# Performance work log

Hardware: AMD Instinct MI355X
Metric: run time of the kernel (lower is better)

Reference implementation:

```python
import jax, jax.numpy as jnp
import numpy as np

MARGIN = 0.2
NEG_SENTINEL = -1e30


def setup_inputs() -> dict:
    key = jax.random.key(0)
    k1, k2 = jax.random.split(key)
    batch_reprs = jax.random.normal(k1, (4096, 128), dtype=jnp.float32)
    batch_labels = jax.random.randint(k2, (4096,), 0, 512, dtype=jnp.int64 if jax.config.jax_enable_x64 else jnp.int32)
    return {"batch_reprs": batch_reprs, "batch_labels": batch_labels}


def _loss(batch_reprs, batch_labels):
    # class match matrix (self-similarity kept, as in original)
    match = (batch_labels[:, None] == batch_labels[None, :]).astype(batch_reprs.dtype)  # [B,B]

    # pairwise euclidean distance (squared=False), sim = -dist
    sq = jnp.sum(batch_reprs * batch_reprs, axis=1)
    d2 = jnp.maximum(sq[:, None] + sq[None, :] - 2.0 * (batch_reprs @ batch_reprs.T), 0.0)
    zero = (d2 == 0.0).astype(batch_reprs.dtype)
    dist = jnp.sqrt(d2 + zero * 1e-16) * (1.0 - zero)
    sim_hat = -dist + (1.0 - match) * MARGIN  # use_margin=True

    # rank positions via double argsort (descending)
    order = jnp.argsort(-sim_hat, axis=1)
    rank = jnp.argsort(order, axis=1).astype(sim_hat.dtype) + 1.0  # [B,B], 1-based ranks

    k = jnp.sum(match, axis=1, keepdims=True)                      # n_pos per row, [B,1]
    fp = (match < 1.0) & (rank <= k)                               # false positives
    fp_num = jnp.sum(fp, axis=1, keepdims=True).astype(sim_hat.dtype)
    fn = (match > 0.0) & (rank > k)                                # false negatives

    n = sim_hat.shape[1]
    # per-row top-(fp_num) false negatives by sim_hat, vectorized via masked sort
    fn_scores = jnp.where(fn, sim_hat, NEG_SENTINEL)
    idx = jnp.argsort(-fn_scores, axis=1)
    fn_sorted = jnp.take_along_axis(sim_hat, idx, axis=1)
    fn_ranks = jnp.take_along_axis(rank, idx, axis=1)
    fn_mask_sorted = jnp.take_along_axis(fn, idx, axis=1)
    sel = (jnp.arange(n)[None, :] < fp_num) & fn_mask_sorted       # top fp_num entries

    # weighted margins (rows with fp_num==0 contribute 0 automatically)
    fp_term = jnp.sum(jnp.where(fp, sim_hat * (0.5 + (k - rank + 1.0) / k * 0.5), 0.0))
    fn_term = jnp.sum(jnp.where(sel, fn_sorted * (0.5 + (fn_ranks - k) / (n - k) * 0.5), 0.0))
    return fp_term - fn_term


def reference(batch_reprs, batch_labels):
    return _loss(batch_reprs, batch_labels)
```

## Files before the change

### kernel.cpp

```cpp
#include <hip/hip_runtime.h>
#include <cstdint>
#include <cstddef>

#define B 4096
#define D 128
#define MARGIN_F 0.2f
#define CW 256
#define ROWS 16
#define SSTR 4104

typedef short bf16x8 __attribute__((ext_vector_type(8)));
typedef float f32x4 __attribute__((ext_vector_type(4)));
typedef uint32_t u32x4 __attribute__((ext_vector_type(4)));

__device__ __forceinline__ uint32_t xform_key(float f) {
    uint32_t u = __float_as_uint(f);
    return u ^ (uint32_t)((((int32_t)u) >> 31) | 0x80000000);
}
__device__ __forceinline__ float unxform16(uint32_t k16) {
    uint32_t u = k16 << 16;
    u = (u & 0x80000000u) ? (u ^ 0x80000000u) : ~u;
    return __uint_as_float(u);
}
__device__ __forceinline__ unsigned short f2bf(float f) {
    uint32_t u = __float_as_uint(f);
    return (unsigned short)((u + 0x7FFFu + ((u >> 16) & 1u)) >> 16);
}

__global__ __launch_bounds__(256) void prep_kernel(const float* __restrict__ R,
                                                   float* __restrict__ sq,
                                                   unsigned short* __restrict__ Rb,
                                                   float* __restrict__ out) {
    if (blockIdx.x == 0 && threadIdx.x == 0) out[0] = 0.0f;
    int wave = threadIdx.x >> 6;
    int lane = threadIdx.x & 63;
    int row  = blockIdx.x * 4 + wave;
    const float2* R2 = (const float2*)R + (size_t)row * (D / 2);
    float2 v = R2[lane];
    ushort2 o; o.x = f2bf(v.x); o.y = f2bf(v.y);
    *(ushort2*)(Rb + (size_t)row * D + lane * 2) = o;
    float s = v.x * v.x + v.y * v.y;
#pragma unroll
    for (int off = 32; off > 0; off >>= 1) s += __shfl_down(s, off);
    if (lane == 0) sq[row] = s;
}

__global__ __launch_bounds__(512) void fused_loss(const unsigned short* __restrict__ Rb,
                                                  const float* __restrict__ sq,
                                                  const int* __restrict__ labels,
                                                  float* __restrict__ out) {
    __shared__ unsigned short S[ROWS * SSTR];
    __shared__ uint32_t cand_c[ROWS][CW];
    __shared__ int cnt[ROWS];

    const int tid  = threadIdx.x;
    const int wid  = tid >> 6, lane = tid & 63;
    const int q    = lane >> 4, t = lane & 15;
    const int r0   = blockIdx.x * ROWS;

    if (tid < ROWS) cnt[tid] = 0;

    bf16x8 af[4];
    const unsigned short* baseA = Rb + (size_t)(r0 + t) * D + q * 8;
#pragma unroll
    for (int kq = 0; kq < 4; ++kq)
        af[kq] = *(const bf16x8*)(baseA + kq * 32);

    float sqa[4]; int la[4];
#pragma unroll
    for (int rr = 0; rr < 4; ++rr) {
        sqa[rr] = sq[r0 + q * 4 + rr];
        la[rr]  = labels[r0 + q * 4 + rr];
    }

    for (int i = 0; i < 32; ++i) {
        const int jt  = wid * 32 + i;
        const int col = jt * 16 + t;
        const unsigned short* baseB = Rb + (size_t)col * D + q * 8;
        bf16x8 bfr[4];
#pragma unroll
        for (int kq = 0; kq < 4; ++kq)
            bfr[kq] = *(const bf16x8*)(baseB + kq * 32);
        f32x4 acc = (f32x4)0.0f;
#pragma unroll
        for (int kq = 0; kq < 4; ++kq)
            acc = __builtin_amdgcn_mfma_f32_16x16x32_bf16(af[kq], bfr[kq], acc, 0, 0, 0);

        const float sqc = sq[col];
        const int   lc  = labels[col];
#pragma unroll
        for (int rr = 0; rr < 4; ++rr) {
            float g  = acc[rr];
            float d2 = fmaxf(sqa[rr] + sqc - 2.0f * g, 0.0f);
            float dist = (d2 > 0.0f) ? sqrtf(d2) : 0.0f;
            float s = -dist + ((la[rr] == lc) ? 0.0f : MARGIN_F);
            uint32_t key = xform_key(s);
            S[(q * 4 + rr) * SSTR + col] = (unsigned short)((key + 0x8000u) >> 16);
        }
    }
    __syncthreads();

    float facc = 0.0f;
    const int4* lv = (const int4*)labels;

    for (int rr2 = 0; rr2 < 2; ++rr2) {
        const int row  = wid * 2 + rr2;
        const int grow = r0 + row;
        const int li   = labels[grow];

        u32x4 kv[8];
#pragma unroll
        for (int qq = 0; qq < 8; ++qq)
            kv[qq] = *(u32x4*)(&S[row * SSTR + (qq * 64 + lane) * 8]);

        uint64_t mbits = 0;
        uint32_t t1 = 0, t2 = 0;
#pragma unroll
        for (int qq = 0; qq < 8; ++qq) {
            const int lb = (qq * 64 + lane) * 2;
            int4 la4 = lv[lb], lc4 = lv[lb + 1];
            uint32_t u[8] = {kv[qq].x & 0xFFFFu, kv[qq].x >> 16,
                             kv[qq].y & 0xFFFFu, kv[qq].y >> 16,
                             kv[qq].z & 0xFFFFu, kv[qq].z >> 16,
                             kv[qq].w & 0xFFFFu, kv[qq].w >> 16};
#pragma unroll
            for (int c = 0; c < 8; ++c) {
                uint32_t mn = min(t1, u[c]);
                t1 = max(t1, u[c]);
                t2 = max(t2, mn);
            }
            mbits |= (uint64_t)(la4.x == li) << (qq * 8 + 0);
            mbits |= (uint64_t)(la4.y == li) << (qq * 8 + 1);
            mbits |= (uint64_t)(la4.z == li) << (qq * 8 + 2);
            mbits |= (uint64_t)(la4.w == li) << (qq * 8 + 3);
            mbits |= (uint64_t)(lc4.x == li) << (qq * 8 + 4);
            mbits |= (uint64_t)(lc4.y == li) << (qq * 8 + 5);
            mbits |= (uint64_t)(lc4.z == li) << (qq * 8 + 6);
            mbits |= (uint64_t)(lc4.w == li) << (qq * 8 + 7);
        }

        int kloc = __popcll(mbits);
#pragma unroll
        for (int off = 32; off > 0; off >>= 1) kloc += __shfl_xor(kloc, off);
        const int k = kloc;
        const float kf = (float)k;

        const int kneed = min(k, 128);
        uint32_t T = 0;
#pragma unroll
        for (int b = 15; b >= 0; --b) {
            uint32_t g = T | (1u << b);
            int c = __popcll(__ballot(t1 >= g)) + __popcll(__ballot(t2 >= g));
            if (c >= kneed) T = g;
        }
        const uint32_t combT = T << 12;

#pragma unroll
        for (int qq = 0; qq < 8; ++qq) {
            uint32_t u[8] = {kv[qq].x & 0xFFFFu, kv[qq].x >> 16,
                             kv[qq].y & 0xFFFFu, kv[qq].y >> 16,
                             kv[qq].z & 0xFFFFu, kv[qq].z >> 16,
                             kv[qq].w & 0xFFFFu, kv[qq].w >> 16};
            int jb = (qq * 64 + lane) * 8;
#pragma unroll
            for (int c = 0; c < 8; ++c) {
                int e = qq * 8 + c;
                uint32_t m = (uint32_t)((mbits >> e) & 1);
                if (u[c] >= T || m) {
                    int p = atomicAdd(&cnt[row], 1);
                    if (p < CW)
                        cand_c[row][p] = (u[c] << 12) | (uint32_t)(4095 - (jb + c)) | (m << 31);
                }
            }
        }
        const int ncand = min(cnt[row], CW);

        for (int s = lane; s < ncand; s += 64) {
            uint32_t cs = cand_c[row][s];
            uint32_t comb = cs & 0x7FFFFFFFu;
            int m = (int)(cs >> 31);
            if (comb >= combT) {
                int c2 = 0;
                for (int c = 0; c < ncand; ++c)
                    c2 += ((cand_c[row][c] & 0x7FFFFFFFu) > comb) ? 1 : 0;
                int rank = 1 + c2;
                float v = unxform16(comb >> 12);
                if (!m && rank <= k)
                    facc += v * (0.5f + ((kf - (float)rank + 1.0f) / kf) * 0.5f);
                else if (m && rank > k)
                    facc -= v * (0.5f + (((float)rank - kf) / (float)(B - k)) * 0.5f);
            }
        }

        uint32_t p0 = 0xFFFFFFFFu, p1 = 0xFFFFFFFFu, p2 = 0xFFFFFFFFu, p3 = 0xFFFFFFFFu;
        int np = 0;
        for (int c = 0; c <= ncand; ++c) {
            bool flushit = (c == ncand);
            if (!flushit) {
                uint32_t cc_ = cand_c[row][c];
                if ((cc_ & 0x80000000u) && (cc_ & 0x7FFFFFFFu) < combT) {
                    uint32_t comb = cc_ & 0x7FFFFFFFu;
                    if (np == 0) p0 = comb; else if (np == 1) p1 = comb;
                    else if (np == 2) p2 = comb; else p3 = comb;
                    ++np;
                    flushit = (np == 4);
                }
            }
            if (flushit && np > 0) {
                int c0 = 0, c1 = 0, c2 = 0, c3 = 0;
#pragma unroll
                for (int qq = 0; qq < 8; ++qq) {
                    uint32_t u[8] = {kv[qq].x & 0xFFFFu, kv[qq].x >> 16,
                                     kv[qq].y & 0xFFFFu, kv[qq].y >> 16,
                                     kv[qq].z & 0xFFFFu, kv[qq].z >> 16,
                                     kv[qq].w & 0xFFFFu, kv[qq].w >> 16};
                    int jb = (qq * 64 + lane) * 8;
#pragma unroll
                    for (int cc = 0; cc < 8; ++cc) {
                        uint32_t comb_e = (u[cc] << 12) | (uint32_t)(4095 - (jb + cc));
                        c0 += (comb_e > p0) ? 1 : 0;
                        c1 += (comb_e > p1) ? 1 : 0;
                        c2 += (comb_e > p2) ? 1 : 0;
                        c3 += (comb_e > p3) ? 1 : 0;
                    }
                }
#pragma unroll
                for (int off = 32; off > 0; off >>= 1) {
                    c0 += __shfl_xor(c0, off); c1 += __shfl_xor(c1, off);
                    c2 += __shfl_xor(c2, off); c3 += __shfl_xor(c3, off);
                }
                if (lane == 0) {
                    int rk[4] = {1 + c0, 1 + c1, 1 + c2, 1 + c3};
                    uint32_t pp[4] = {p0, p1, p2, p3};
                    for (int ii = 0; ii < np; ++ii) {
                        float v = unxform16(pp[ii] >> 12);
                        facc -= v * (0.5f + (((float)rk[ii] - kf) / (float)(B - k)) * 0.5f);
                    }
                }
                p0 = p1 = p2 = p3 = 0xFFFFFFFFu;
                np = 0;
            }
        }
    }

#pragma unroll
    for (int off = 32; off > 0; off >>= 1) facc += __shfl_xor(facc, off);
    if (lane == 0) atomicAdd(out, facc);
}

extern "C" void kernel_launch(void* const* d_in, const int* in_sizes, int n_in,
                              void* d_out, int out_size, void* d_ws, size_t ws_size,
                              hipStream_t stream) {
    const float* R      = (const float*)d_in[0];
    const int*   labels = (const int*)d_in[1];
    float* out = (float*)d_out;

    float*          sq = (float*)d_ws;
    unsigned short* Rb = (unsigned short*)((char*)d_ws + 16 * 1024);

    hipLaunchKernelGGL(prep_kernel, dim3(B / 4), dim3(256), 0, stream, R, sq, Rb, out);
    hipLaunchKernelGGL(fused_loss, dim3(B / ROWS), dim3(512), 0, stream,
                       Rb, sq, labels, out);
}
```

Before: 135.7 us.

## Register-blocked candidate ranking and ballot-based batching of false-negative rank queries

The candidate rank pass is rewritten so each lane holds four candidates in registers and scans the shared candidate list once with vectorized 128-bit loads, rather than doing a scalar scan per candidate. The candidate buffer is zeroed first so the list can be padded to a multiple of 8 without reading garbage. Low-score false negatives are now collected with wave ballots and shuffles and ranked eight at a time against the full row, instead of being found by a serial scan and ranked four at a time. This cuts LDS traffic and the number of full-row passes, at the cost of higher register pressure and a small zero-initialization step.

```diff
diff --git a/kernel.cpp b/kernel.cpp
--- a/kernel.cpp
+++ b/kernel.cpp
@@ -58,6 +58,12 @@
     const int q    = lane >> 4, t = lane & 15;
     const int r0   = blockIdx.x * ROWS;
 
+    {
+        uint32_t* cz = &cand_c[0][0];
+#pragma unroll
+        for (int c = 0; c < (ROWS * CW) / 512; ++c)
+            cz[tid + c * 512] = 0u;
+    }
     if (tid < ROWS) cnt[tid] = 0;
 
     bf16x8 af[4];
@@ -175,72 +181,108 @@
         }
         const int ncand = min(cnt[row], CW);
 
-        for (int s = lane; s < ncand; s += 64) {
-            uint32_t cs = cand_c[row][s];
-            uint32_t comb = cs & 0x7FFFFFFFu;
-            int m = (int)(cs >> 31);
-            if (comb >= combT) {
-                int c2 = 0;
-                for (int c = 0; c < ncand; ++c)
-                    c2 += ((cand_c[row][c] & 0x7FFFFFFFu) > comb) ? 1 : 0;
-                int rank = 1 + c2;
-                float v = unxform16(comb >> 12);
-                if (!m && rank <= k)
+        uint32_t cr0 = cand_c[row][lane];
+        uint32_t cr1 = cand_c[row][lane + 64];
+        uint32_t cr2 = cand_c[row][lane + 128];
+        uint32_t cr3 = cand_c[row][lane + 192];
+        uint32_t mycomb[4] = {cr0 & 0x7FFFFFFFu, cr1 & 0x7FFFFFFFu,
+                              cr2 & 0x7FFFFFFFu, cr3 & 0x7FFFFFFFu};
+        int mym[4]  = {(int)(cr0 >> 31), (int)(cr1 >> 31),
+                       (int)(cr2 >> 31), (int)(cr3 >> 31)};
+        int myok[4] = {lane < ncand, lane + 64 < ncand,
+                       lane + 128 < ncand, lane + 192 < ncand};
+        int myc[4]  = {0, 0, 0, 0};
+
+        const int npad = (ncand + 7) & ~7;
+        for (int c0i = 0; c0i < npad; c0i += 8) {
+            u32x4 a = *(const u32x4*)&cand_c[row][c0i];
+            u32x4 b = *(const u32x4*)&cand_c[row][c0i + 4];
+            uint32_t vv[8] = {a.x, a.y, a.z, a.w, b.x, b.y, b.z, b.w};
+#pragma unroll
+            for (int e = 0; e < 8; ++e) {
+                uint32_t vm = vv[e] & 0x7FFFFFFFu;
+#pragma unroll
+                for (int j = 0; j < 4; ++j)
+                    myc[j] += (vm > mycomb[j]) ? 1 : 0;
+            }
+        }
+
+#pragma unroll
+        for (int j = 0; j < 4; ++j) {
+            if (myok[j] && mycomb[j] >= combT) {
+                int rank = 1 + myc[j];
+                float v = unxform16(mycomb[j] >> 12);
+                if (!mym[j] && rank <= k)
                     facc += v * (0.5f + ((kf - (float)rank + 1.0f) / kf) * 0.5f);
-                else if (m && rank > k)
+                else if (mym[j] && rank > k)
                     facc -= v * (0.5f + (((float)rank - kf) / (float)(B - k)) * 0.5f);
             }
         }
 
         uint32_t p0 = 0xFFFFFFFFu, p1 = 0xFFFFFFFFu, p2 = 0xFFFFFFFFu, p3 = 0xFFFFFFFFu;
+        uint32_t p4 = 0xFFFFFFFFu, p5 = 0xFFFFFFFFu, p6 = 0xFFFFFFFFu, p7 = 0xFFFFFFFFu;
+
+        auto flush8 = [&](int npv) {
+            int c0 = 0, c1 = 0, c2 = 0, c3 = 0, c4 = 0, c5 = 0, c6 = 0, c7 = 0;
+#pragma unroll
+            for (int qq = 0; qq < 8; ++qq) {
+                uint32_t u[8] = {kv[qq].x & 0xFFFFu, kv[qq].x >> 16,
+                                 kv[qq].y & 0xFFFFu, kv[qq].y >> 16,
+                                 kv[qq].z & 0xFFFFu, kv[qq].z >> 16,
+                                 kv[qq].w & 0xFFFFu, kv[qq].w >> 16};
+                int jb = (qq * 64 + lane) * 8;
+#pragma unroll
+                for (int cc = 0; cc < 8; ++cc) {
+                    uint32_t ce = (u[cc] << 12) | (uint32_t)(4095 - (jb + cc));
+                    c0 += (ce > p0) ? 1 : 0;  c1 += (ce > p1) ? 1 : 0;
+                    c2 += (ce > p2) ? 1 : 0;  c3 += (ce > p3) ? 1 : 0;
+                    c4 += (ce > p4) ? 1 : 0;  c5 += (ce > p5) ? 1 : 0;
+                    c6 += (ce > p6) ? 1 : 0;  c7 += (ce > p7) ? 1 : 0;
+                }
+            }
+#pragma unroll
+            for (int off = 32; off > 0; off >>= 1) {
+                c0 += __shfl_xor(c0, off); c1 += __shfl_xor(c1, off);
+                c2 += __shfl_xor(c2, off); c3 += __shfl_xor(c3, off);
+                c4 += __shfl_xor(c4, off); c5 += __shfl_xor(c5, off);
+                c6 += __shfl_xor(c6, off); c7 += __shfl_xor(c7, off);
+            }
+            if (lane == 0) {
+                if (npv > 0) facc -= unxform16(p0 >> 12) * (0.5f + (((float)(1 + c0) - kf) / (float)(B - k)) * 0.5f);
+                if (npv > 1) facc -= unxform16(p1 >> 12) * (0.5f + (((float)(1 + c1) - kf) / (float)(B - k)) * 0.5f);
+                if (npv > 2) facc -= unxform16(p2 >> 12) * (0.5f + (((float)(1 + c2) - kf) / (float)(B - k)) * 0.5f);
+                if (npv > 3) facc -= unxform16(p3 >> 12) * (0.5f + (((float)(1 + c3) - kf) / (float)(B - k)) * 0.5f);
+                if (npv > 4) facc -= unxform16(p4 >> 12) * (0.5f + (((float)(1 + c4) - kf) / (float)(B - k)) * 0.5f);
+                if (npv > 5) facc -= unxform16(p5 >> 12) * (0.5f + (((float)(1 + c5) - kf) / (float)(B - k)) * 0.5f);
+                if (npv > 6) facc -= unxform16(p6 >> 12) * (0.5f + (((float)(1 + c6) - kf) / (float)(B - k)) * 0.5f);
+                if (npv > 7) facc -= unxform16(p7 >> 12) * (0.5f + (((float)(1 + c7) - kf) / (float)(B - k)) * 0.5f);
+            }
+            p0 = p1 = p2 = p3 = p4 = p5 = p6 = p7 = 0xFFFFFFFFu;
+        };
+
         int np = 0;
-        for (int c = 0; c <= ncand; ++c) {
-            bool flushit = (c == ncand);
-            if (!flushit) {
-                uint32_t cc_ = cand_c[row][c];
-                if ((cc_ & 0x80000000u) && (cc_ & 0x7FFFFFFFu) < combT) {
-                    uint32_t comb = cc_ & 0x7FFFFFFFu;
-                    if (np == 0) p0 = comb; else if (np == 1) p1 = comb;
-                    else if (np == 2) p2 = comb; else p3 = comb;
-                    ++np;
-                    flushit = (np == 4);
+#pragma unroll
+        for (int j = 0; j < 4; ++j) {
+            uint64_t mg = __ballot(myok[j] && mym[j] && (mycomb[j] < combT));
+            while (mg) {
+                int src = __ffsll((unsigned long long)mg) - 1;
+                mg &= mg - 1;
+                uint32_t pc;
+                if (j == 0)      pc = __shfl(mycomb[0], src);
+                else if (j == 1) pc = __shfl(mycomb[1], src);
+                else if (j == 2) pc = __shfl(mycomb[2], src);
+                else             pc = __shfl(mycomb[3], src);
+                switch (np) {
+                    case 0: p0 = pc; break; case 1: p1 = pc; break;
+                    case 2: p2 = pc; break; case 3: p3 = pc; break;
+                    case 4: p4 = pc; break; case 5: p5 = pc; break;
+                    case 6: p6 = pc; break; default: p7 = pc; break;
                 }
-            }
-            if (flushit && np > 0) {
-                int c0 = 0, c1 = 0, c2 = 0, c3 = 0;
-#pragma unroll
-                for (int qq = 0; qq < 8; ++qq) {
-                    uint32_t u[8] = {kv[qq].x & 0xFFFFu, kv[qq].x >> 16,
-                                     kv[qq].y & 0xFFFFu, kv[qq].y >> 16,
-                                     kv[qq].z & 0xFFFFu, kv[qq].z >> 16,
-                                     kv[qq].w & 0xFFFFu, kv[qq].w >> 16};
-                    int jb = (qq * 64 + lane) * 8;
-#pragma unroll
-                    for (int cc = 0; cc < 8; ++cc) {
-                        uint32_t comb_e = (u[cc] << 12) | (uint32_t)(4095 - (jb + cc));
-                        c0 += (comb_e > p0) ? 1 : 0;
-                        c1 += (comb_e > p1) ? 1 : 0;
-                        c2 += (comb_e > p2) ? 1 : 0;
-                        c3 += (comb_e > p3) ? 1 : 0;
-                    }
-                }
-#pragma unroll
-                for (int off = 32; off > 0; off >>= 1) {
-                    c0 += __shfl_xor(c0, off); c1 += __shfl_xor(c1, off);
-                    c2 += __shfl_xor(c2, off); c3 += __shfl_xor(c3, off);
-                }
-                if (lane == 0) {
-                    int rk[4] = {1 + c0, 1 + c1, 1 + c2, 1 + c3};
-                    uint32_t pp[4] = {p0, p1, p2, p3};
-                    for (int ii = 0; ii < np; ++ii) {
-                        float v = unxform16(pp[ii] >> 12);
-                        facc -= v * (0.5f + (((float)rk[ii] - kf) / (float)(B - k)) * 0.5f);
-                    }
-                }
-                p0 = p1 = p2 = p3 = 0xFFFFFFFFu;
-                np = 0;
-            }
-        }
+                ++np;
+                if (np == 8) { flush8(8); np = 0; }
+            }
+        }
+        if (np > 0) flush8(np);
     }
 
 #pragma unroll
```

New measurement: 166.5 us. 1.23x slower.
